# Kernel tuning notes

Hardware: AMD Instinct MI355X
Metric: run time of the kernel (lower is better)

## Reference

```python
import jax, jax.numpy as jnp
import numpy as np


def setup_inputs() -> dict:
    key = jax.random.key(0)
    kx, k1, k2 = jax.random.split(key, 3)
    x = jax.random.normal(kx, (2, 1, 256, 256), dtype=jnp.float32)
    # keras 'random_normal' initializer: stddev=0.05
    w1 = jax.random.normal(k1, (1,), dtype=jnp.float32) * 0.05
    w2 = jax.random.normal(k2, (1,), dtype=jnp.float32) * 0.05
    return {"x": x, "w1": w1, "w2": w2}


def reference(x, w1, w2):
    # x: [B, 1, H, W] (channels_first, single channel as implied by kernel in_ch=1)
    # SAME padding (TF: pad_left = (k-1)//2 = (i+1)//2). Each conv is equivalent to
    #   y_i[w] = w1 * x[w - (i+1)//2] + w2 * x[w + (i+2)//2]   (zero outside [0, W))
    # Outputs are concatenated on axis=1 -> [B, W, H, W].
    B, C, H, W = x.shape
    x2 = x[:, 0]  # [B, H, W]
    i = jnp.arange(W)[:, None]   # shift index -> output channel
    w = jnp.arange(W)[None, :]   # spatial position
    idx1 = w - (i + 1) // 2      # [W_i, W_w]
    idx2 = w + (i + 2) // 2      # [W_i, W_w]
    m1 = ((idx1 >= 0) & (idx1 < W)).astype(x.dtype)
    m2 = ((idx2 >= 0) & (idx2 < W)).astype(x.dtype)
    g1 = jnp.take(x2, jnp.clip(idx1, 0, W - 1), axis=2)  # [B, H, W_i, W_w]
    g2 = jnp.take(x2, jnp.clip(idx2, 0, W - 1), axis=2)  # [B, H, W_i, W_w]
    out = w1[0] * g1 * m1 + w2[0] * g2 * m2
    return jnp.transpose(out, (0, 2, 1, 3))  # [B, W_i, H, W_w]
```

## Files before the change

kernel.cpp:

```cpp
#include <hip/hip_runtime.h>


__global__ __launch_bounds__(256) void ConvolutionalOverlap_kernel(
    const float* __restrict__ x,
    const float* __restrict__ w1p,
    const float* __restrict__ w2p,
    float* __restrict__ out,
    int total4)
{
    const float w1 = w1p[0];
    const float w2 = w2p[0];
    const int stride = gridDim.x * blockDim.x;

    for (int idx = blockIdx.x * blockDim.x + threadIdx.x; idx < total4;
         idx += stride) {
        const int w4 = idx & 63;
        const int h  = (idx >> 6)  & 255;
        const int i  = (idx >> 14) & 255;
        const int b  = idx >> 22;

        const int s1 = (i + 1) >> 1;
        const int s2 = (i + 2) >> 1;

        const float* __restrict__ row = x + (b << 16) + (h << 8);

        const int w0 = w4 << 2;
        float4 o;
        float* op = reinterpret_cast<float*>(&o);
        #pragma unroll
        for (int j = 0; j < 4; ++j) {
            const int w = w0 + j;
            float v = 0.0f;
            if (w >= s1)      v  = w1 * row[w - s1];
            if (w + s2 < 256) v += w2 * row[w + s2];
            op[j] = v;
        }
        reinterpret_cast<float4*>(out)[idx] = o;
    }
}

extern "C" void kernel_launch(void* const* d_in, const int* in_sizes, int n_in,
                              void* d_out, int out_size, void* d_ws, size_t ws_size,
                              hipStream_t stream) {
    const float* x  = (const float*)d_in[0];
    const float* w1 = (const float*)d_in[1];
    const float* w2 = (const float*)d_in[2];
    float* out = (float*)d_out;

    const int total4 = out_size / 4;
    const int block = 256;
    const int grid = 2048;

    hipLaunchKernelGGL(ConvolutionalOverlap_kernel, dim3(grid), dim3(block), 0,
                       stream, x, w1, w2, out, total4);
}
```

Measured before the change: 167.9 us.

## Stage input row in zero-padded LDS and assign blocks per (b,h,channel-chunk)

Each block now loads one input row into a zero-padded shared-memory buffer and produces 64 output channels for that row. Reads come from LDS with no boundary branches, and the grid-stride loop is replaced by a fixed block-to-(batch,row,chunk) mapping. The kernel is dominated by writing the 128 MB output, so the gain depends on whether the store pattern stays as efficient. Stores are now strided by channel (i<<16) across iterations, and the LDS reads are unaligned, which can cause bank conflicts.

Measured after the change: 156.5 us. -6.8%, faster.

```diff
diff --git a/kernel.cpp b/kernel.cpp
--- a/kernel.cpp
+++ b/kernel.cpp
@@ -5,37 +5,46 @@
     const float* __restrict__ x,
     const float* __restrict__ w1p,
     const float* __restrict__ w2p,
-    float* __restrict__ out,
-    int total4)
+    float* __restrict__ out)
 {
+    __shared__ float lds[512];
+
+    const int bid = blockIdx.x;
+    const int b   = bid >> 10;
+    const int h   = (bid >> 2) & 255;
+    const int ic  = bid & 3;
+    const int t   = threadIdx.x;
+
+    if (t < 128) lds[t] = 0.0f;
+    else         lds[256 + t] = 0.0f;
+    lds[128 + t] = x[(b << 16) + (h << 8) + t];
+    __syncthreads();
+
     const float w1 = w1p[0];
     const float w2 = w2p[0];
-    const int stride = gridDim.x * blockDim.x;
 
-    for (int idx = blockIdx.x * blockDim.x + threadIdx.x; idx < total4;
-         idx += stride) {
-        const int w4 = idx & 63;
-        const int h  = (idx >> 6)  & 255;
-        const int i  = (idx >> 14) & 255;
-        const int b  = idx >> 22;
+    const int lane = t & 63;
+    const int wv   = t >> 6;
+    const int w0   = lane << 2;
 
+    #pragma unroll 4
+    for (int it = 0; it < 16; ++it) {
+        const int i  = (ic << 6) + (it << 2) + wv;
         const int s1 = (i + 1) >> 1;
         const int s2 = (i + 2) >> 1;
 
-        const float* __restrict__ row = x + (b << 16) + (h << 8);
+        const int a1 = 128 - s1 + w0;
+        const int a2 = 128 + s2 + w0;
 
-        const int w0 = w4 << 2;
         float4 o;
-        float* op = reinterpret_cast<float*>(&o);
-        #pragma unroll
-        for (int j = 0; j < 4; ++j) {
-            const int w = w0 + j;
-            float v = 0.0f;
-            if (w >= s1)      v  = w1 * row[w - s1];
-            if (w + s2 < 256) v += w2 * row[w + s2];
-            op[j] = v;
-        }
-        reinterpret_cast<float4*>(out)[idx] = o;
+        o.x = w1 * lds[a1]     + w2 * lds[a2];
+        o.y = w1 * lds[a1 + 1] + w2 * lds[a2 + 1];
+        o.z = w1 * lds[a1 + 2] + w2 * lds[a2 + 2];
+        o.w = w1 * lds[a1 + 3] + w2 * lds[a2 + 3];
+
+        float4* dst = reinterpret_cast<float4*>(
+            out + (b << 24) + (i << 16) + (h << 8) + w0);
+        *dst = o;
     }
 }
 
@@ -47,10 +56,9 @@
     const float* w2 = (const float*)d_in[2];
     float* out = (float*)d_out;
 
-    const int total4 = out_size / 4;
+    const int grid  = 2 * 256 * 4;
     const int block = 256;
-    const int grid = 2048;
 
     hipLaunchKernelGGL(ConvolutionalOverlap_kernel, dim3(grid), dim3(block), 0,
-                       stream, x, w1, w2, out, total4);
+                       stream, x, w1, w2, out);
 }
```

## Zero-pad input rows in a prepass and use branchless vector loads with nontemporal stores

Applied to the files above, without the earlier changes.

A small prepass kernel copies each input row into a 512-wide zero-padded buffer in workspace. The main kernel can then drop the boundary checks and read both shifted windows with unaligned 16-byte loads. The main kernel also switches from a grid-stride loop to a fixed per-block mapping over (batch, shift, row chunk), and it writes the 128 MB output with nontemporal stores. The cost is an extra kernel launch and a small workspace round trip, and the path depends on the workspace being large enough.

New measurement: 143.3 us. -14.7%, faster.

```diff
diff --git a/kernel.cpp b/kernel.cpp
--- a/kernel.cpp
+++ b/kernel.cpp
@@ -1,41 +1,67 @@
 #include <hip/hip_runtime.h>
 
 
+typedef float v4f __attribute__((ext_vector_type(4)));
+
+__global__ __launch_bounds__(256) void pad_kernel(
+    const float* __restrict__ x, float* __restrict__ xpad)
+{
+    const int f = blockIdx.x * 256 + threadIdx.x;
+    const int r = f >> 7;
+    const int c = f & 127;
+
+    v4f v;
+    if (c < 32 || c >= 96) {
+        v = (v4f){0.f, 0.f, 0.f, 0.f};
+    } else {
+        v = *reinterpret_cast<const v4f*>(x + (r << 8) + ((c - 32) << 2));
+    }
+    *reinterpret_cast<v4f*>(xpad + (f << 2)) = v;
+}
+
 __global__ __launch_bounds__(256) void ConvolutionalOverlap_kernel(
-    const float* __restrict__ x,
+    const float* __restrict__ xpad,
     const float* __restrict__ w1p,
     const float* __restrict__ w2p,
-    float* __restrict__ out,
-    int total4)
+    float* __restrict__ out)
 {
+    const int bid = blockIdx.x;
+    const int b   = bid >> 10;
+    const int i   = (bid >> 2) & 255;
+    const int hc  = bid & 3;
+
     const float w1 = w1p[0];
     const float w2 = w2p[0];
-    const int stride = gridDim.x * blockDim.x;
 
-    for (int idx = blockIdx.x * blockDim.x + threadIdx.x; idx < total4;
-         idx += stride) {
-        const int w4 = idx & 63;
-        const int h  = (idx >> 6)  & 255;
-        const int i  = (idx >> 14) & 255;
-        const int b  = idx >> 22;
+    const int s1 = (i + 1) >> 1;
+    const int s2 = (i + 2) >> 1;
 
-        const int s1 = (i + 1) >> 1;
-        const int s2 = (i + 2) >> 1;
+    const int t  = threadIdx.x;
+    const int w4 = t & 63;
+    const int hs = t >> 6;
+    const int w0 = w4 << 2;
 
-        const float* __restrict__ row = x + (b << 16) + (h << 8);
+    const float* __restrict__ padb = xpad + (b << 17);
+    float* __restrict__ outb = out + (b << 24) + (i << 16) + (hc << 14);
 
-        const int w0 = w4 << 2;
-        float4 o;
-        float* op = reinterpret_cast<float*>(&o);
-        #pragma unroll
-        for (int j = 0; j < 4; ++j) {
-            const int w = w0 + j;
-            float v = 0.0f;
-            if (w >= s1)      v  = w1 * row[w - s1];
-            if (w + s2 < 256) v += w2 * row[w + s2];
-            op[j] = v;
-        }
-        reinterpret_cast<float4*>(out)[idx] = o;
+    #pragma unroll
+    for (int it = 0; it < 16; ++it) {
+        const int hl = (it << 2) + hs;
+        const float* __restrict__ rowp = padb + (hl << 9) + ((hc << 6) << 9 >> 0) ;
+        const float* __restrict__ row = padb + (((hc << 6) + hl) << 9);
+
+        const float* p1 = row + 128 + w0 - s1;
+        const float* p2 = row + 128 + w0 + s2;
+
+        v4f a, c;
+        __builtin_memcpy(&a, p1, 16);
+        __builtin_memcpy(&c, p2, 16);
+
+        v4f o = w1 * a + w2 * c;
+
+        v4f* dst = reinterpret_cast<v4f*>(outb + (hl << 8) + w0);
+        __builtin_nontemporal_store(o, dst);
+        (void)rowp;
     }
 }
 
@@ -45,12 +71,10 @@
     const float* x  = (const float*)d_in[0];
     const float* w1 = (const float*)d_in[1];
     const float* w2 = (const float*)d_in[2];
-    float* out = (float*)d_out;
+    float* out  = (float*)d_out;
+    float* xpad = (float*)d_ws;
 
-    const int total4 = out_size / 4;
-    const int block = 256;
-    const int grid = 2048;
-
-    hipLaunchKernelGGL(ConvolutionalOverlap_kernel, dim3(grid), dim3(block), 0,
-                       stream, x, w1, w2, out, total4);
+    hipLaunchKernelGGL(pad_kernel, dim3(256), dim3(256), 0, stream, x, xpad);
+    hipLaunchKernelGGL(ConvolutionalOverlap_kernel, dim3(2048), dim3(256), 0,
+                       stream, xpad, w1, w2, out);
 }
```
